# Kernel optimization log

Measured on AMD Instinct MI355X. Metric: run time of the kernel, lower is better.

## Reference

```python
import jax, jax.numpy as jnp
import numpy as np

EPS = 1e-6          # module eps for denominator
KERNEL_EPS = 1e-4   # performer softmax_kernel numerical eps


def softmax_kernel(data, projection):
    # data: [n, l, h, e]; projection: [m, e] -> features [n, l, h, m]
    d = data.shape[-1]
    m = projection.shape[0]
    data_normalizer = d ** -0.25
    ratio = m ** -0.5
    data_dash = jnp.einsum('nlhe,me->nlhm', data * data_normalizer, projection)
    diag_data = (0.5 * (data_normalizer ** 2)) * jnp.sum(data * data, axis=-1, keepdims=True)
    # numerically stable exp with per-row max subtraction
    data_dash = ratio * (jnp.exp(data_dash - diag_data - jnp.max(data_dash, axis=-1, keepdims=True)) + KERNEL_EPS)
    return data_dash


def _gaussian_orthogonal_random_matrix(nb_rows, nb_cols, seed=0):
    rng = np.random.default_rng(seed)
    blocks = []
    for _ in range(int(np.ceil(nb_rows / nb_cols))):
        q, _ = np.linalg.qr(rng.standard_normal((nb_cols, nb_cols)))
        blocks.append(q.T)
    proj = np.concatenate(blocks, axis=0)[:nb_rows]
    # scaling=0: chi-distributed row multipliers
    multiplier = np.linalg.norm(rng.standard_normal((nb_rows, nb_cols)), axis=1)
    return (multiplier[:, None] * proj).astype(np.float32)


def setup_inputs() -> dict:
    n, l, h, e = 2, 2048, 8, 64
    nb_features = l  # module: nb_features = l when l >= e
    key = jax.random.key(0)
    kq, kk, kv = jax.random.split(key, 3)
    queries = jax.random.normal(kq, (n, l, h, e), jnp.float32)
    keys = jax.random.normal(kk, (n, l, h, e), jnp.float32)
    values = jax.random.normal(kv, (n, l, h, e), jnp.float32)
    projection = jnp.asarray(_gaussian_orthogonal_random_matrix(nb_features, e))
    return {"queries": queries, "keys": keys, "values": values, "projection": projection}


def reference(queries, keys, values, projection):
    # Performer linear attention, batched (bi=None) branch
    q = softmax_kernel(queries, projection)   # [n, l, h, m]
    k = softmax_kernel(keys, projection)      # [n, l, h, m]
    kv = jnp.einsum('nshm,nshe->nhem', k, values)              # [n, h, e, m]
    z = 1.0 / (jnp.einsum('nlhm,nhm->nlh', q, k.sum(axis=1)) + EPS)  # [n, l, h]
    v = jnp.einsum('nlhm,nhem,nlh->nlhe', q, kv, z)             # [n, l, h, e]
    return v
```

## Files before the change

kernel.cpp:

```cpp
#include <hip/hip_runtime.h>


#define LL 2048
#define HH 8
#define MM 2048
#define ROWSTR 512

#define NORMC 0.35355339059327373f
#define RATIO 0.022097086912079608f
#define KEPS 1e-4f
#define REPS (RATIO * KEPS)
#define EPSD 1e-6f

#define KVSPLIT 2097152
#define RSPLIT 32768

typedef __attribute__((ext_vector_type(8))) short short8;
typedef __attribute__((ext_vector_type(4))) float f32x4;

#define MFMA(a, b, c) __builtin_amdgcn_mfma_f32_16x16x32_bf16((a), (b), (c), 0, 0, 0)

__device__ __forceinline__ unsigned short f2bf(float f) {
    union { float f; unsigned int u; } v; v.f = f;
    unsigned int r = v.u + 0x7fffu + ((v.u >> 16) & 1u);
    return (unsigned short)(r >> 16);
}
__device__ __forceinline__ float bf2f(unsigned short u) {
    union { unsigned int ui; float f; } v; v.ui = ((unsigned int)u) << 16; return v.f;
}
__device__ __forceinline__ unsigned int pk2(float lo, float hi) {
    return __builtin_amdgcn_perm(__float_as_uint(hi), __float_as_uint(lo), 0x07060302u);
}

template <bool BF16>
__device__ __forceinline__ void tile_load(const void* src, size_t base, size_t rstride,
                                          int t, uint4& A, uint4& B) {
    const int row = t >> 2, c16 = (t & 3) * 16;
    if (BF16) {
        const unsigned short* p = (const unsigned short*)src + base + (size_t)row * rstride + c16;
        A = *(const uint4*)p;
        B = *(const uint4*)(p + 8);
    } else {
        const float* p = (const float*)src + base + (size_t)row * rstride + c16;
        float4 f0 = ((const float4*)p)[0], f1 = ((const float4*)p)[1];
        float4 f2 = ((const float4*)p)[2], f3 = ((const float4*)p)[3];
        A.x = pk2(f0.x, f0.y); A.y = pk2(f0.z, f0.w);
        A.z = pk2(f1.x, f1.y); A.w = pk2(f1.z, f1.w);
        B.x = pk2(f2.x, f2.y); B.y = pk2(f2.z, f2.w);
        B.z = pk2(f3.x, f3.y); B.w = pk2(f3.z, f3.w);
    }
}
__device__ __forceinline__ void tile_store(unsigned short D[64][72], int t, uint4 A, uint4 B) {
    const int row = t >> 2, c16 = (t & 3) * 16;
    *(uint4*)&D[row][c16] = A;
    *(uint4*)&D[row][c16 + 8] = B;
}

template <bool BF16>
__device__ __forceinline__ void vt_load(const void* V, size_t base, int t, uint4& A, uint4& B) {
    const int s0 = (t & 31) * 2, e0 = (t >> 5) * 8;
    if (BF16) {
        const unsigned short* p = (const unsigned short*)V + base + (size_t)s0 * ROWSTR + e0;
        A = *(const uint4*)p;
        B = *(const uint4*)(p + ROWSTR);
    } else {
        const float* p = (const float*)V + base + (size_t)s0 * ROWSTR + e0;
        float4 f0 = ((const float4*)p)[0], f1 = ((const float4*)p)[1];
        const float* q = p + ROWSTR;
        float4 g0 = ((const float4*)q)[0], g1 = ((const float4*)q)[1];
        A.x = pk2(f0.x, f0.y); A.y = pk2(f0.z, f0.w);
        A.z = pk2(f1.x, f1.y); A.w = pk2(f1.z, f1.w);
        B.x = pk2(g0.x, g0.y); B.y = pk2(g0.z, g0.w);
        B.z = pk2(g1.x, g1.y); B.w = pk2(g1.z, g1.w);
    }
}
__device__ __forceinline__ void vt_store(unsigned short VT[64][72], int t, uint4 A, uint4 B) {
    const int s0 = (t & 31) * 2, e0 = (t >> 5) * 8;
    const unsigned ua[4] = {A.x, A.y, A.z, A.w}, ub[4] = {B.x, B.y, B.z, B.w};
    #pragma unroll
    for (int i = 0; i < 4; ++i) {
        *(unsigned*)&VT[e0 + 2 * i][s0] = (ua[i] & 0xFFFFu) | (ub[i] << 16);
        *(unsigned*)&VT[e0 + 2 * i + 1][s0] = (ua[i] >> 16) | (ub[i] & 0xFFFF0000u);
    }
}

__device__ __forceinline__ void kv2_load(const float* kvf01, size_t base, int t, float4 R[8]) {
    const int m0 = (t & 31) * 2, e0 = (t >> 5) * 8;
    const float* p = kvf01 + base + (size_t)m0 * 64 + e0;
    R[0] = ((const float4*)p)[0];        R[1] = ((const float4*)p)[1];
    R[2] = ((const float4*)(p + 64))[0]; R[3] = ((const float4*)(p + 64))[1];
    const float* q = p + KVSPLIT;
    R[4] = ((const float4*)q)[0];        R[5] = ((const float4*)q)[1];
    R[6] = ((const float4*)(q + 64))[0]; R[7] = ((const float4*)(q + 64))[1];
}
__device__ __forceinline__ void kv2_store(unsigned short D[64][72], int t, const float4 R[8]) {
    const int m0 = (t & 31) * 2, e0 = (t >> 5) * 8;
    const float r0[8] = {R[0].x + R[4].x, R[0].y + R[4].y, R[0].z + R[4].z, R[0].w + R[4].w,
                         R[1].x + R[5].x, R[1].y + R[5].y, R[1].z + R[5].z, R[1].w + R[5].w};
    const float r1[8] = {R[2].x + R[6].x, R[2].y + R[6].y, R[2].z + R[6].z, R[2].w + R[6].w,
                         R[3].x + R[7].x, R[3].y + R[7].y, R[3].z + R[7].z, R[3].w + R[7].w};
    #pragma unroll
    for (int i = 0; i < 8; ++i)
        *(unsigned*)&D[e0 + i][m0] = (unsigned)f2bf(r0[i]) | ((unsigned)f2bf(r1[i]) << 16);
}

__global__ void LinearAttention_15985868276494_detect(const unsigned short* __restrict__ P,
                                                      float* __restrict__ flag) {
    if (threadIdx.x == 0) {
        int sane = 1;
        #pragma unroll
        for (int i = 0; i < 16; ++i) {
            const unsigned e = (P[2 * i] >> 7) & 0xFF;
            if (e < 101 || e > 141) sane = 0;
        }
        *flag = sane ? 1.0f : 0.0f;
    }
}

template <bool BF16>
__device__ void stats_impl(const void* X, const void* P, float* cws,
                           unsigned short Xs[64][72], unsigned short Ps[2][64][72],
                           float* diag_s) {
    const int t = threadIdx.x;
    const int w = t >> 6, ln = t & 15, quad = (t >> 4) & 3;
    const int row_base = blockIdx.x * 64;

    {
        uint4 xa, xb;
        tile_load<BF16>(X, (size_t)row_base * 64, 64, t, xa, xb);
        tile_store(Xs, t, xa, xb);
        uint4 pa, pb;
        tile_load<BF16>(P, 0, 64, t, pa, pb);
        tile_store(Ps[0], t, pa, pb);
    }
    __syncthreads();
    if (t < 64) {
        float s2 = 0.f;
        #pragma unroll
        for (int c = 0; c < 64; c += 8) {
            uint4 u = *(const uint4*)&Xs[t][c];
            const unsigned int ua[4] = {u.x, u.y, u.z, u.w};
            #pragma unroll
            for (int i = 0; i < 4; ++i) {
                float lo = bf2f((unsigned short)(ua[i] & 0xFFFF));
                float hi = bf2f((unsigned short)(ua[i] >> 16));
                s2 = fmaf(lo, lo, s2); s2 = fmaf(hi, hi, s2);
            }
        }
        diag_s[t] = s2;
    }
    const short8 xb0 = *(const short8*)&Xs[16 * w + ln][quad * 8];
    const short8 xb1 = *(const short8*)&Xs[16 * w + ln][32 + quad * 8];

    uint4 pfa, pfb;
    tile_load<BF16>(P, (size_t)64 * 64, 64, t, pfa, pfb);

    float rmax = -3.0e38f;
    for (int mt = 0; mt < 32; ++mt) {
        const int cur = mt & 1;
        __syncthreads();
        if (mt + 1 < 32) {
            tile_store(Ps[cur ^ 1], t, pfa, pfb);
            if (mt + 2 < 32)
                tile_load<BF16>(P, (size_t)((mt + 2) * 64) * 64, 64, t, pfa, pfb);
        }
        #pragma unroll
        for (int ms = 0; ms < 4; ++ms) {
            f32x4 acc = {0.f, 0.f, 0.f, 0.f};
            acc = MFMA(*(const short8*)&Ps[cur][16 * ms + ln][quad * 8], xb0, acc);
            acc = MFMA(*(const short8*)&Ps[cur][16 * ms + ln][32 + quad * 8], xb1, acc);
            rmax = fmaxf(rmax, fmaxf(fmaxf(acc[0], acc[1]), fmaxf(acc[2], acc[3])));
        }
    }
    rmax = fmaxf(rmax, __shfl_xor(rmax, 16));
    rmax = fmaxf(rmax, __shfl_xor(rmax, 32));
    __syncthreads();
    if ((t & 63) < 16) {
        const int row = 16 * w + ln;
        const int rg = row_base + row;
        const int n = rg >> 14, l = (rg >> 3) & 2047, h = rg & 7;
        cws[(size_t)((n << 3) | h) * LL + l] =
            NORMC * rmax + (0.5f * NORMC * NORMC) * diag_s[row];
    }
}

__global__ __launch_bounds__(256) void LinearAttention_15985868276494_stats(
        const void* K, const void* Q, const void* P, const float* flag,
        float* c_k, float* c_q) {
    __shared__ unsigned short Xs[64][72];
    __shared__ unsigned short Ps[2][64][72];
    __shared__ float diag_s[64];
    const void* X = (blockIdx.y == 0) ? K : Q;
    float* cws = (blockIdx.y == 0) ? c_k : c_q;
    if (*flag != 0.f) stats_impl<true>(X, P, cws, Xs, Ps, diag_s);
    else stats_impl<false>(X, P, cws, Xs, Ps, diag_s);
}

template <bool BF16>
__device__ void kv_impl(const void* K, const void* V, const void* P, const float* cws,
                        float* kvf01, float* ksum01,
                        unsigned short Ks[2][64][72], unsigned short VT[2][64][72],
                        unsigned short Ps[64][72], unsigned short FT[64][72],
                        float cks[2][64]) {
    const int t = threadIdx.x;
    const int w = t >> 6, ln = t & 15, quad = (t >> 4) & 3;
    const int mt = blockIdx.x, nh = blockIdx.y, sp = blockIdx.z;
    const int n = nh >> 3, h = nh & 7;
    const size_t xbase = (size_t)n * (LL * ROWSTR) + (size_t)h * 64;
    const int st0 = sp * 16;

    {
        uint4 pa, pb;
        tile_load<BF16>(P, (size_t)(mt * 64) * 64, 64, t, pa, pb);
        tile_store(Ps, t, pa, pb);
    }
    uint4 kA, kB, vA, vB;
    float ckr = 0.f;
    tile_load<BF16>(K, xbase + (size_t)(st0 * 64) * ROWSTR, ROWSTR, t, kA, kB);
    vt_load<BF16>(V, xbase + (size_t)(st0 * 64) * ROWSTR, t, vA, vB);
    if (t < 64) ckr = cws[(size_t)nh * LL + st0 * 64 + t];
    tile_store(Ks[0], t, kA, kB);
    vt_store(VT[0], t, vA, vB);
    if (t < 64) cks[0][t] = ckr;
    tile_load<BF16>(K, xbase + (size_t)((st0 + 1) * 64) * ROWSTR, ROWSTR, t, kA, kB);
    vt_load<BF16>(V, xbase + (size_t)((st0 + 1) * 64) * ROWSTR, t, vA, vB);
    if (t < 64) ckr = cws[(size_t)nh * LL + (st0 + 1) * 64 + t];
    __syncthreads();

    const short8 pb0 = *(const short8*)&Ps[16 * w + ln][quad * 8];
    const short8 pb1 = *(const short8*)&Ps[16 * w + ln][32 + quad * 8];
    f32x4 akv[4] = {{0.f, 0.f, 0.f, 0.f}, {0.f, 0.f, 0.f, 0.f},
                    {0.f, 0.f, 0.f, 0.f}, {0.f, 0.f, 0.f, 0.f}};
    f32x4 aks = {0.f, 0.f, 0.f, 0.f};
    const short8 ones = {0x3F80, 0x3F80, 0x3F80, 0x3F80, 0x3F80, 0x3F80, 0x3F80, 0x3F80};

    for (int i = 0; i < 16; ++i) {
        const int cur = i & 1;
        if (i + 1 < 16) {
            tile_store(Ks[cur ^ 1], t, kA, kB);
            vt_store(VT[cur ^ 1], t, vA, vB);
            if (t < 64) cks[cur ^ 1][t] = ckr;
            if (i + 2 < 16) {
                const int st = st0 + i + 2;
                tile_load<BF16>(K, xbase + (size_t)(st * 64) * ROWSTR, ROWSTR, t, kA, kB);
                vt_load<BF16>(V, xbase + (size_t)(st * 64) * ROWSTR, t, vA, vB);
                if (t < 64) ckr = cws[(size_t)nh * LL + st * 64 + t];
            }
        }
        #pragma unroll
        for (int ss = 0; ss < 4; ++ss) {
            f32x4 acc = {0.f, 0.f, 0.f, 0.f};
            acc = MFMA(*(const short8*)&Ks[cur][16 * ss + ln][quad * 8], pb0, acc);
            acc = MFMA(*(const short8*)&Ks[cur][16 * ss + ln][32 + quad * 8], pb1, acc);
            const float4 c4 = *(const float4*)&cks[cur][16 * ss + 4 * quad];
            const float ca[4] = {c4.x, c4.y, c4.z, c4.w};
            float f[4];
            #pragma unroll
            for (int j = 0; j < 4; ++j) {
                const float arg = fminf(fmaf(acc[j], NORMC, -ca[j]), 0.f);
                f[j] = fmaf(__expf(arg), RATIO, REPS);
            }
            uint2 o; o.x = pk2(f[0], f[1]); o.y = pk2(f[2], f[3]);
            *(uint2*)&FT[16 * w + ln][16 * ss + 4 * quad] = o;
        }
        #pragma unroll
        for (int k = 0; k < 2; ++k) {
            const short8 af = *(const short8*)&FT[16 * w + ln][32 * k + quad * 8];
            aks = MFMA(af, ones, aks);
            #pragma unroll
            for (int es = 0; es < 4; ++es)
                akv[es] = MFMA(af, *(const short8*)&VT[cur][16 * es + ln][32 * k + quad * 8],
                               akv[es]);
        }
        __syncthreads();
    }
    float* kvfp = kvf01 + (size_t)sp * KVSPLIT + (size_t)nh * (MM * 64);
    #pragma unroll
    for (int r = 0; r < 4; ++r) {
        const int m = mt * 64 + 16 * w + 4 * quad + r;
        #pragma unroll
        for (int es = 0; es < 4; ++es)
            kvfp[(size_t)m * 64 + 16 * es + ln] = akv[es][r];
        if (ln == 0)
            ksum01[(size_t)sp * RSPLIT + (size_t)nh * MM + m] = aks[r];
    }
}

__global__ __launch_bounds__(256) void LinearAttention_15985868276494_kv(
        const void* K, const void* V, const void* P, const float* flag,
        const float* cws, float* kvf01, float* ksum01) {
    __shared__ unsigned short Ks[2][64][72];
    __shared__ unsigned short VT[2][64][72];
    __shared__ unsigned short Ps[64][72];
    __shared__ unsigned short FT[64][72];
    __shared__ float cks[2][64];
    if (*flag != 0.f) kv_impl<true>(K, V, P, cws, kvf01, ksum01, Ks, VT, Ps, FT, cks);
    else kv_impl<false>(K, V, P, cws, kvf01, ksum01, Ks, VT, Ps, FT, cks);
}

__global__ __launch_bounds__(256) void LinearAttention_15985868276494_reduce(
        const float* __restrict__ kvf01, const float* __restrict__ ksum01,
        unsigned short* __restrict__ kvT, float* __restrict__ ksum) {
    __shared__ unsigned short T[64][72];
    const int t = threadIdx.x;
    const int mt = blockIdx.x, nh = blockIdx.y;
    float4 R[8];
    kv2_load(kvf01, (size_t)nh * (MM * 64) + (size_t)(mt * 64) * 64, t, R);
    kv2_store(T, t, R);
    if (t < 64)
        ksum[(size_t)nh * MM + mt * 64 + t] =
            ksum01[(size_t)nh * MM + mt * 64 + t] +
            ksum01[RSPLIT + (size_t)nh * MM + mt * 64 + t];
    __syncthreads();
    const int e = t >> 2, c = (t & 3) * 16;
    uint4 a = *(const uint4*)&T[e][c];
    uint4 b = *(const uint4*)&T[e][c + 8];
    unsigned short* dst = kvT + ((size_t)nh * 64 + e) * MM + mt * 64 + c;
    *(uint4*)dst = a;
    *(uint4*)(dst + 8) = b;
}

template <bool BF16>
__device__ void out_impl(const void* Q, const void* P, const float* cqw,
                         const unsigned short* kvT, const float* ksum, void* out,
                         unsigned short Qs[64][72], unsigned short Ps[2][64][72],
                         unsigned short KVs[2][64][72], unsigned short Fs[64][72],
                         unsigned short kss[2][72]) {
    const int t = threadIdx.x;
    const int w = t >> 6, ln = t & 15, quad = (t >> 4) & 3;
    const int lb = blockIdx.x, nh = blockIdx.y;
    const int n = nh >> 3, h = nh & 7;
    const size_t qbase = (size_t)n * (LL * ROWSTR) + (size_t)h * 64 + (size_t)(lb * 64) * ROWSTR;
    const size_t kvbase = (size_t)nh * (size_t)(64 * MM);

    {
        uint4 qa, qb;
        tile_load<BF16>(Q, qbase, ROWSTR, t, qa, qb);
        tile_store(Qs, t, qa, qb);
    }
    uint4 pA, pB, kA, kB;
    float ksr = 0.f;
    tile_load<BF16>(P, 0, 64, t, pA, pB);
    tile_load<true>(kvT, kvbase, MM, t, kA, kB);
    if (t < 64) ksr = ksum[(size_t)nh * MM + t];
    tile_store(Ps[0], t, pA, pB);
    tile_store(KVs[0], t, kA, kB);
    if (t < 64) kss[0][t] = f2bf(ksr);
    tile_load<BF16>(P, (size_t)64 * 64, 64, t, pA, pB);
    tile_load<true>(kvT, kvbase + 64, MM, t, kA, kB);
    if (t < 64) ksr = ksum[(size_t)nh * MM + 64 + t];
    __syncthreads();

    const short8 qb0 = *(const short8*)&Qs[16 * w + ln][quad * 8];
    const short8 qb1 = *(const short8*)&Qs[16 * w + ln][32 + quad * 8];
    const float cq = cqw[(size_t)nh * LL + lb * 64 + 16 * w + ln];

    f32x4 ao[4] = {{0.f, 0.f, 0.f, 0.f}, {0.f, 0.f, 0.f, 0.f},
                   {0.f, 0.f, 0.f, 0.f}, {0.f, 0.f, 0.f, 0.f}};
    f32x4 ad = {0.f, 0.f, 0.f, 0.f};

    for (int mt = 0; mt < 32; ++mt) {
        const int cur = mt & 1;
        if (mt + 1 < 32) {
            tile_store(Ps[cur ^ 1], t, pA, pB);
            tile_store(KVs[cur ^ 1], t, kA, kB);
            if (t < 64) kss[cur ^ 1][t] = f2bf(ksr);
            if (mt + 2 < 32) {
                tile_load<BF16>(P, (size_t)((mt + 2) * 64) * 64, 64, t, pA, pB);
                tile_load<true>(kvT, kvbase + (mt + 2) * 64, MM, t, kA, kB);
                if (t < 64) ksr = ksum[(size_t)nh * MM + (mt + 2) * 64 + t];
            }
        }
        #pragma unroll
        for (int ms = 0; ms < 4; ++ms) {
            f32x4 acc = {0.f, 0.f, 0.f, 0.f};
            acc = MFMA(*(const short8*)&Ps[cur][16 * ms + ln][quad * 8], qb0, acc);
            acc = MFMA(*(const short8*)&Ps[cur][16 * ms + ln][32 + quad * 8], qb1, acc);
            float f[4];
            #pragma unroll
            for (int j = 0; j < 4; ++j) {
                const float arg = fminf(fmaf(acc[j], NORMC, -cq), 0.f);
                f[j] = fmaf(__expf(arg), RATIO, REPS);
            }
            uint2 o; o.x = pk2(f[0], f[1]); o.y = pk2(f[2], f[3]);
            *(uint2*)&Fs[16 * w + ln][16 * ms + 4 * quad] = o;
        }
        #pragma unroll
        for (int k = 0; k < 2; ++k) {
            const short8 af = *(const short8*)&Fs[16 * w + ln][32 * k + quad * 8];
            const short8 bs = *(const short8*)&kss[cur][32 * k + quad * 8];
            ad = MFMA(af, bs, ad);
            #pragma unroll
            for (int es = 0; es < 4; ++es)
                ao[es] = MFMA(af, *(const short8*)&KVs[cur][16 * es + ln][32 * k + quad * 8],
                              ao[es]);
        }
        __syncthreads();
    }
    float z[4];
    #pragma unroll
    for (int r = 0; r < 4; ++r) z[r] = 1.0f / (ad[r] + EPSD);
    #pragma unroll
    for (int r = 0; r < 4; ++r) {
        const int l = lb * 64 + 16 * w + 4 * quad + r;
        const size_t rowoff = ((size_t)(n * LL + l) * HH + h) * 64;
        #pragma unroll
        for (int es = 0; es < 4; ++es) {
            const float val = ao[es][r] * z[r];
            if (BF16) ((unsigned short*)out)[rowoff + 16 * es + ln] = f2bf(val);
            else ((float*)out)[rowoff + 16 * es + ln] = val;
        }
    }
}

__global__ __launch_bounds__(256) void LinearAttention_15985868276494_out(
        const void* Q, const void* P, const float* flag, const float* cqw,
        const unsigned short* kvT, const float* ksum, void* out) {
    __shared__ unsigned short Qs[64][72];
    __shared__ unsigned short Ps[2][64][72];
    __shared__ unsigned short KVs[2][64][72];
    __shared__ unsigned short Fs[64][72];
    __shared__ unsigned short kss[2][72];
    if (*flag != 0.f) out_impl<true>(Q, P, cqw, kvT, ksum, out, Qs, Ps, KVs, Fs, kss);
    else out_impl<false>(Q, P, cqw, kvT, ksum, out, Qs, Ps, KVs, Fs, kss);
}

extern "C" void kernel_launch(void* const* d_in, const int* in_sizes, int n_in,
                              void* d_out, int out_size, void* d_ws, size_t ws_size,
                              hipStream_t stream) {
    const void* Q = d_in[0];
    const void* K = d_in[1];
    const void* V = d_in[2];
    const void* P = d_in[3];

    float* W = (float*)d_ws;
    float* flag = W;
    float* c_k = W + 16;
    float* c_q = c_k + 32768;
    float* ksum01 = c_q + 32768;
    float* kvf01 = ksum01 + 2 * RSPLIT;
    float* ksumW = kvf01 + 2 * KVSPLIT;
    unsigned short* kvTW = (unsigned short*)(ksumW + RSPLIT);

    LinearAttention_15985868276494_detect<<<1, 64, 0, stream>>>(
        (const unsigned short*)P, flag);
    LinearAttention_15985868276494_stats<<<dim3(512, 2), 256, 0, stream>>>(
        K, Q, P, flag, c_k, c_q);
    LinearAttention_15985868276494_kv<<<dim3(32, 16, 2), 256, 0, stream>>>(
        K, V, P, flag, c_k, kvf01, ksum01);
    LinearAttention_15985868276494_reduce<<<dim3(32, 16), 256, 0, stream>>>(
        kvf01, ksum01, kvTW, ksumW);
    LinearAttention_15985868276494_out<<<dim3(32, 16), 256, 0, stream>>>(
        Q, P, flag, c_q, kvTW, ksumW, d_out);
}
```

Measured before the change: 214.6 us.

## Switch all GEMM stages to 32x32x16 MFMA with register-shuffled feature fragments

Replaces the 16x16x32 bf16 MFMA tiling with 32x32x16 MFMA across the stats, kv and output kernels. The exp feature tile now stays in registers and is passed to the next MFMA through lane-xor shuffles instead of a shared-memory round trip. The stats kernel processes 128 rows per block, and the output kernel splits work across waves, reducing partial results through shared memory in an epilogue that writes vectorized stores. Launch bounds, dynamic shared memory sizes and the reduce grid change to match. The aim is fewer MFMA issues, fewer LDS accesses and fewer barriers, in exchange for more register pressure and a more complex cross-wave reduction.

```diff
diff --git a/kernel.cpp b/kernel.cpp
--- a/kernel.cpp
+++ b/kernel.cpp
@@ -16,20 +16,26 @@
 #define RSPLIT 32768
 
 typedef __attribute__((ext_vector_type(8))) short short8;
-typedef __attribute__((ext_vector_type(4))) float f32x4;
-
-#define MFMA(a, b, c) __builtin_amdgcn_mfma_f32_16x16x32_bf16((a), (b), (c), 0, 0, 0)
-
+typedef __attribute__((ext_vector_type(16))) float f32x16;
+
+#define MFMA32(a, b, c) __builtin_amdgcn_mfma_f32_32x32x16_bf16((a), (b), (c), 0, 0, 0)
+
+__device__ __forceinline__ f32x16 zero16() {
+    f32x16 v;
+    #pragma unroll
+    for (int i = 0; i < 16; ++i) v[i] = 0.f;
+    return v;
+}
 __device__ __forceinline__ unsigned short f2bf(float f) {
     union { float f; unsigned int u; } v; v.f = f;
     unsigned int r = v.u + 0x7fffu + ((v.u >> 16) & 1u);
     return (unsigned short)(r >> 16);
 }
+__device__ __forceinline__ unsigned int pk2(float lo, float hi) {
+    return __builtin_amdgcn_perm(__float_as_uint(hi), __float_as_uint(lo), 0x07060302u);
+}
 __device__ __forceinline__ float bf2f(unsigned short u) {
     union { unsigned int ui; float f; } v; v.ui = ((unsigned int)u) << 16; return v.f;
-}
-__device__ __forceinline__ unsigned int pk2(float lo, float hi) {
-    return __builtin_amdgcn_perm(__float_as_uint(hi), __float_as_uint(lo), 0x07060302u);
 }
 
 template <bool BF16>
@@ -50,10 +56,10 @@
         B.z = pk2(f3.x, f3.y); B.w = pk2(f3.z, f3.w);
     }
 }
-__device__ __forceinline__ void tile_store(unsigned short D[64][72], int t, uint4 A, uint4 B) {
+__device__ __forceinline__ void tile_store72(unsigned short* D, int t, uint4 A, uint4 B) {
     const int row = t >> 2, c16 = (t & 3) * 16;
-    *(uint4*)&D[row][c16] = A;
-    *(uint4*)&D[row][c16 + 8] = B;
+    *(uint4*)&D[row * 72 + c16] = A;
+    *(uint4*)&D[row * 72 + c16 + 8] = B;
 }
 
 template <bool BF16>
@@ -74,34 +80,27 @@
         B.z = pk2(g1.x, g1.y); B.w = pk2(g1.z, g1.w);
     }
 }
-__device__ __forceinline__ void vt_store(unsigned short VT[64][72], int t, uint4 A, uint4 B) {
+__device__ __forceinline__ void vt_store72(unsigned short* VT, int t, uint4 A, uint4 B) {
     const int s0 = (t & 31) * 2, e0 = (t >> 5) * 8;
     const unsigned ua[4] = {A.x, A.y, A.z, A.w}, ub[4] = {B.x, B.y, B.z, B.w};
     #pragma unroll
     for (int i = 0; i < 4; ++i) {
-        *(unsigned*)&VT[e0 + 2 * i][s0] = (ua[i] & 0xFFFFu) | (ub[i] << 16);
-        *(unsigned*)&VT[e0 + 2 * i + 1][s0] = (ua[i] >> 16) | (ub[i] & 0xFFFF0000u);
-    }
-}
-
-__device__ __forceinline__ void kv2_load(const float* kvf01, size_t base, int t, float4 R[8]) {
-    const int m0 = (t & 31) * 2, e0 = (t >> 5) * 8;
-    const float* p = kvf01 + base + (size_t)m0 * 64 + e0;
-    R[0] = ((const float4*)p)[0];        R[1] = ((const float4*)p)[1];
-    R[2] = ((const float4*)(p + 64))[0]; R[3] = ((const float4*)(p + 64))[1];
-    const float* q = p + KVSPLIT;
-    R[4] = ((const float4*)q)[0];        R[5] = ((const float4*)q)[1];
-    R[6] = ((const float4*)(q + 64))[0]; R[7] = ((const float4*)(q + 64))[1];
-}
-__device__ __forceinline__ void kv2_store(unsigned short D[64][72], int t, const float4 R[8]) {
-    const int m0 = (t & 31) * 2, e0 = (t >> 5) * 8;
-    const float r0[8] = {R[0].x + R[4].x, R[0].y + R[4].y, R[0].z + R[4].z, R[0].w + R[4].w,
-                         R[1].x + R[5].x, R[1].y + R[5].y, R[1].z + R[5].z, R[1].w + R[5].w};
-    const float r1[8] = {R[2].x + R[6].x, R[2].y + R[6].y, R[2].z + R[6].z, R[2].w + R[6].w,
-                         R[3].x + R[7].x, R[3].y + R[7].y, R[3].z + R[7].z, R[3].w + R[7].w};
-    #pragma unroll
-    for (int i = 0; i < 8; ++i)
-        *(unsigned*)&D[e0 + i][m0] = (unsigned)f2bf(r0[i]) | ((unsigned)f2bf(r1[i]) << 16);
+        *(unsigned*)&VT[(e0 + 2 * i) * 72 + s0] = (ua[i] & 0xFFFFu) | (ub[i] << 16);
+        *(unsigned*)&VT[(e0 + 2 * i + 1) * 72 + s0] = (ua[i] >> 16) | (ub[i] & 0xFFFF0000u);
+    }
+}
+
+__device__ __forceinline__ short8 xfrag(const unsigned int pd[8], int cp, int hi) {
+    const unsigned int s0 = hi ? pd[4 * cp + 0] : pd[4 * cp + 2];
+    const unsigned int s1 = hi ? pd[4 * cp + 1] : pd[4 * cp + 3];
+    const unsigned int r0 = (unsigned int)__shfl_xor((int)s0, 32);
+    const unsigned int r1 = (unsigned int)__shfl_xor((int)s1, 32);
+    union { unsigned int u[4]; short8 s; } v;
+    v.u[0] = hi ? r0 : pd[4 * cp + 0];
+    v.u[1] = hi ? r1 : pd[4 * cp + 1];
+    v.u[2] = hi ? pd[4 * cp + 2] : r0;
+    v.u[3] = hi ? pd[4 * cp + 3] : r1;
+    return v.s;
 }
 
 __global__ void LinearAttention_15985868276494_detect(const unsigned short* __restrict__ P,
@@ -119,127 +118,149 @@
 
 template <bool BF16>
 __device__ void stats_impl(const void* X, const void* P, float* cws,
-                           unsigned short Xs[64][72], unsigned short Ps[2][64][72],
-                           float* diag_s) {
+                           unsigned short* Xs, unsigned short* Ps, float* red) {
     const int t = threadIdx.x;
-    const int w = t >> 6, ln = t & 15, quad = (t >> 4) & 3;
-    const int row_base = blockIdx.x * 64;
-
-    {
-        uint4 xa, xb;
-        tile_load<BF16>(X, (size_t)row_base * 64, 64, t, xa, xb);
-        tile_store(Xs, t, xa, xb);
-        uint4 pa, pb;
-        tile_load<BF16>(P, 0, 64, t, pa, pb);
-        tile_store(Ps[0], t, pa, pb);
-    }
+    const int w = t >> 6, ln = t & 31, hi = (t >> 5) & 1;
+    const int row_base = blockIdx.x * 128;
+
+    uint4 a0, b0, a1, b1;
+    tile_load<BF16>(X, (size_t)row_base * 64, 64, t, a0, b0);
+    tile_store72(Xs, t, a0, b0);
+    tile_load<BF16>(X, (size_t)(row_base + 64) * 64, 64, t, a1, b1);
+    tile_store72(Xs + 64 * 72, t, a1, b1);
+    tile_load<BF16>(P, 0, 64, t, a0, b0);
+    tile_store72(Ps, t, a0, b0);
+    tile_load<BF16>(P, (size_t)64 * 64, 64, t, a1, b1);
+    tile_store72(Ps + 64 * 72, t, a1, b1);
+    uint4 pA0, pB0, pA1, pB1;
+    tile_load<BF16>(P, (size_t)128 * 64, 64, t, pA0, pB0);
+    tile_load<BF16>(P, (size_t)192 * 64, 64, t, pA1, pB1);
     __syncthreads();
-    if (t < 64) {
+
+    short8 xb[4][4];
+    #pragma unroll
+    for (int xs = 0; xs < 4; ++xs)
+        #pragma unroll
+        for (int c = 0; c < 4; ++c)
+            xb[xs][c] = *(const short8*)&Xs[(32 * xs + ln) * 72 + 16 * c + 8 * hi];
+
+    float rmax4[4] = {-3e38f, -3e38f, -3e38f, -3e38f};
+    for (int mt = 0; mt < 16; ++mt) {
+        const int cur = mt & 1;
+        unsigned short* Pc = Ps + cur * (128 * 72);
+        if (mt + 1 < 16) {
+            unsigned short* Pn = Ps + (cur ^ 1) * (128 * 72);
+            tile_store72(Pn, t, pA0, pB0);
+            tile_store72(Pn + 64 * 72, t, pA1, pB1);
+            if (mt + 2 < 16) {
+                tile_load<BF16>(P, (size_t)((mt + 2) * 128) * 64, 64, t, pA0, pB0);
+                tile_load<BF16>(P, (size_t)((mt + 2) * 128 + 64) * 64, 64, t, pA1, pB1);
+            }
+        }
+        #pragma unroll
+        for (int xs = 0; xs < 4; ++xs) {
+            f32x16 acc = zero16();
+            #pragma unroll
+            for (int c = 0; c < 4; ++c) {
+                const short8 af = *(const short8*)&Pc[(32 * w + ln) * 72 + 16 * c + 8 * hi];
+                acc = MFMA32(af, xb[xs][c], acc);
+            }
+            float m = acc[0];
+            #pragma unroll
+            for (int r = 1; r < 16; ++r) m = fmaxf(m, acc[r]);
+            rmax4[xs] = fmaxf(rmax4[xs], m);
+        }
+        __syncthreads();
+    }
+    #pragma unroll
+    for (int xs = 0; xs < 4; ++xs) {
+        const float m = fmaxf(rmax4[xs], __shfl_xor(rmax4[xs], 32));
+        if (hi == 0) red[w * 128 + xs * 32 + ln] = m;
+    }
+    __syncthreads();
+    if (t < 128) {
+        const float rm = fmaxf(fmaxf(red[t], red[128 + t]), fmaxf(red[256 + t], red[384 + t]));
         float s2 = 0.f;
         #pragma unroll
         for (int c = 0; c < 64; c += 8) {
-            uint4 u = *(const uint4*)&Xs[t][c];
+            uint4 u = *(const uint4*)&Xs[t * 72 + c];
             const unsigned int ua[4] = {u.x, u.y, u.z, u.w};
             #pragma unroll
             for (int i = 0; i < 4; ++i) {
-                float lo = bf2f((unsigned short)(ua[i] & 0xFFFF));
-                float hi = bf2f((unsigned short)(ua[i] >> 16));
-                s2 = fmaf(lo, lo, s2); s2 = fmaf(hi, hi, s2);
-            }
-        }
-        diag_s[t] = s2;
-    }
-    const short8 xb0 = *(const short8*)&Xs[16 * w + ln][quad * 8];
-    const short8 xb1 = *(const short8*)&Xs[16 * w + ln][32 + quad * 8];
-
-    uint4 pfa, pfb;
-    tile_load<BF16>(P, (size_t)64 * 64, 64, t, pfa, pfb);
-
-    float rmax = -3.0e38f;
-    for (int mt = 0; mt < 32; ++mt) {
-        const int cur = mt & 1;
-        __syncthreads();
-        if (mt + 1 < 32) {
-            tile_store(Ps[cur ^ 1], t, pfa, pfb);
-            if (mt + 2 < 32)
-                tile_load<BF16>(P, (size_t)((mt + 2) * 64) * 64, 64, t, pfa, pfb);
-        }
-        #pragma unroll
-        for (int ms = 0; ms < 4; ++ms) {
-            f32x4 acc = {0.f, 0.f, 0.f, 0.f};
-            acc = MFMA(*(const short8*)&Ps[cur][16 * ms + ln][quad * 8], xb0, acc);
-            acc = MFMA(*(const short8*)&Ps[cur][16 * ms + ln][32 + quad * 8], xb1, acc);
-            rmax = fmaxf(rmax, fmaxf(fmaxf(acc[0], acc[1]), fmaxf(acc[2], acc[3])));
-        }
-    }
-    rmax = fmaxf(rmax, __shfl_xor(rmax, 16));
-    rmax = fmaxf(rmax, __shfl_xor(rmax, 32));
-    __syncthreads();
-    if ((t & 63) < 16) {
-        const int row = 16 * w + ln;
-        const int rg = row_base + row;
+                const float lo = bf2f((unsigned short)(ua[i] & 0xFFFF));
+                const float hv = bf2f((unsigned short)(ua[i] >> 16));
+                s2 = fmaf(lo, lo, s2); s2 = fmaf(hv, hv, s2);
+            }
+        }
+        const int rg = row_base + t;
         const int n = rg >> 14, l = (rg >> 3) & 2047, h = rg & 7;
-        cws[(size_t)((n << 3) | h) * LL + l] =
-            NORMC * rmax + (0.5f * NORMC * NORMC) * diag_s[row];
-    }
-}
-
-__global__ __launch_bounds__(256) void LinearAttention_15985868276494_stats(
+        cws[(size_t)((n << 3) | h) * LL + l] = NORMC * rm + (0.5f * NORMC * NORMC) * s2;
+    }
+}
+
+__global__ __launch_bounds__(256, 2) void LinearAttention_15985868276494_stats(
         const void* K, const void* Q, const void* P, const float* flag,
         float* c_k, float* c_q) {
-    __shared__ unsigned short Xs[64][72];
-    __shared__ unsigned short Ps[2][64][72];
-    __shared__ float diag_s[64];
+    __shared__ unsigned short Xs[128 * 72];
+    __shared__ unsigned short Ps[2 * 128 * 72];
+    __shared__ float red[512];
     const void* X = (blockIdx.y == 0) ? K : Q;
     float* cws = (blockIdx.y == 0) ? c_k : c_q;
-    if (*flag != 0.f) stats_impl<true>(X, P, cws, Xs, Ps, diag_s);
-    else stats_impl<false>(X, P, cws, Xs, Ps, diag_s);
+    if (*flag != 0.f) stats_impl<true>(X, P, cws, Xs, Ps, red);
+    else stats_impl<false>(X, P, cws, Xs, Ps, red);
 }
 
 template <bool BF16>
 __device__ void kv_impl(const void* K, const void* V, const void* P, const float* cws,
-                        float* kvf01, float* ksum01,
-                        unsigned short Ks[2][64][72], unsigned short VT[2][64][72],
-                        unsigned short Ps[64][72], unsigned short FT[64][72],
-                        float cks[2][64]) {
+                        float* kvf01, float* ksum01, char* smem) {
+    unsigned short* Ks = (unsigned short*)smem;
+    unsigned short* VT = (unsigned short*)(smem + 18432);
+    unsigned short* Ps = (unsigned short*)(smem + 36864);
+    float* cks = (float*)(smem + 46080);
+    float* fin = (float*)smem;
+
     const int t = threadIdx.x;
-    const int w = t >> 6, ln = t & 15, quad = (t >> 4) & 3;
+    const int w = t >> 6, ln = t & 31, hi = (t >> 5) & 1;
+    const int sstrip = w & 1, mstrip = w >> 1;
     const int mt = blockIdx.x, nh = blockIdx.y, sp = blockIdx.z;
     const int n = nh >> 3, h = nh & 7;
     const size_t xbase = (size_t)n * (LL * ROWSTR) + (size_t)h * 64;
     const int st0 = sp * 16;
 
     {
-        uint4 pa, pb;
-        tile_load<BF16>(P, (size_t)(mt * 64) * 64, 64, t, pa, pb);
-        tile_store(Ps, t, pa, pb);
-    }
-    uint4 kA, kB, vA, vB;
-    float ckr = 0.f;
+        uint4 pa, pbv;
+        tile_load<BF16>(P, (size_t)(mt * 64) * 64, 64, t, pa, pbv);
+        tile_store72(Ps, t, pa, pbv);
+    }
+    uint4 kA, kB, vA, vB; float ckr = 0.f;
     tile_load<BF16>(K, xbase + (size_t)(st0 * 64) * ROWSTR, ROWSTR, t, kA, kB);
     vt_load<BF16>(V, xbase + (size_t)(st0 * 64) * ROWSTR, t, vA, vB);
     if (t < 64) ckr = cws[(size_t)nh * LL + st0 * 64 + t];
-    tile_store(Ks[0], t, kA, kB);
-    vt_store(VT[0], t, vA, vB);
-    if (t < 64) cks[0][t] = ckr;
+    tile_store72(Ks, t, kA, kB);
+    vt_store72(VT, t, vA, vB);
+    if (t < 64) cks[t] = ckr;
     tile_load<BF16>(K, xbase + (size_t)((st0 + 1) * 64) * ROWSTR, ROWSTR, t, kA, kB);
     vt_load<BF16>(V, xbase + (size_t)((st0 + 1) * 64) * ROWSTR, t, vA, vB);
     if (t < 64) ckr = cws[(size_t)nh * LL + (st0 + 1) * 64 + t];
     __syncthreads();
 
-    const short8 pb0 = *(const short8*)&Ps[16 * w + ln][quad * 8];
-    const short8 pb1 = *(const short8*)&Ps[16 * w + ln][32 + quad * 8];
-    f32x4 akv[4] = {{0.f, 0.f, 0.f, 0.f}, {0.f, 0.f, 0.f, 0.f},
-                    {0.f, 0.f, 0.f, 0.f}, {0.f, 0.f, 0.f, 0.f}};
-    f32x4 aks = {0.f, 0.f, 0.f, 0.f};
+    short8 pb[4];
+    #pragma unroll
+    for (int c = 0; c < 4; ++c)
+        pb[c] = *(const short8*)&Ps[(32 * mstrip + ln) * 72 + 16 * c + 8 * hi];
     const short8 ones = {0x3F80, 0x3F80, 0x3F80, 0x3F80, 0x3F80, 0x3F80, 0x3F80, 0x3F80};
+
+    f32x16 akv0 = zero16(), akv1 = zero16(), aks = zero16();
 
     for (int i = 0; i < 16; ++i) {
         const int cur = i & 1;
+        unsigned short* Kc = Ks + cur * 4608;
+        unsigned short* Vc = VT + cur * 4608;
+        const float* cc = cks + cur * 64;
         if (i + 1 < 16) {
-            tile_store(Ks[cur ^ 1], t, kA, kB);
-            vt_store(VT[cur ^ 1], t, vA, vB);
-            if (t < 64) cks[cur ^ 1][t] = ckr;
+            tile_store72(Ks + (cur ^ 1) * 4608, t, kA, kB);
+            vt_store72(VT + (cur ^ 1) * 4608, t, vA, vB);
+            if (t < 64) cks[(cur ^ 1) * 64 + t] = ckr;
             if (i + 2 < 16) {
                 const int st = st0 + i + 2;
                 tile_load<BF16>(K, xbase + (size_t)(st * 64) * ROWSTR, ROWSTR, t, kA, kB);
@@ -247,182 +268,248 @@
                 if (t < 64) ckr = cws[(size_t)nh * LL + st * 64 + t];
             }
         }
-        #pragma unroll
-        for (int ss = 0; ss < 4; ++ss) {
-            f32x4 acc = {0.f, 0.f, 0.f, 0.f};
-            acc = MFMA(*(const short8*)&Ks[cur][16 * ss + ln][quad * 8], pb0, acc);
-            acc = MFMA(*(const short8*)&Ks[cur][16 * ss + ln][32 + quad * 8], pb1, acc);
-            const float4 c4 = *(const float4*)&cks[cur][16 * ss + 4 * quad];
+        f32x16 D = zero16();
+        #pragma unroll
+        for (int c = 0; c < 4; ++c) {
+            const short8 af = *(const short8*)&Kc[(32 * sstrip + ln) * 72 + 16 * c + 8 * hi];
+            D = MFMA32(af, pb[c], D);
+        }
+        unsigned int pd[8];
+        #pragma unroll
+        for (int g = 0; g < 4; ++g) {
+            const float4 c4 = *(const float4*)&cc[32 * sstrip + 8 * g + 4 * hi];
             const float ca[4] = {c4.x, c4.y, c4.z, c4.w};
             float f[4];
             #pragma unroll
-            for (int j = 0; j < 4; ++j) {
-                const float arg = fminf(fmaf(acc[j], NORMC, -ca[j]), 0.f);
-                f[j] = fmaf(__expf(arg), RATIO, REPS);
-            }
-            uint2 o; o.x = pk2(f[0], f[1]); o.y = pk2(f[2], f[3]);
-            *(uint2*)&FT[16 * w + ln][16 * ss + 4 * quad] = o;
-        }
-        #pragma unroll
-        for (int k = 0; k < 2; ++k) {
-            const short8 af = *(const short8*)&FT[16 * w + ln][32 * k + quad * 8];
-            aks = MFMA(af, ones, aks);
-            #pragma unroll
-            for (int es = 0; es < 4; ++es)
-                akv[es] = MFMA(af, *(const short8*)&VT[cur][16 * es + ln][32 * k + quad * 8],
-                               akv[es]);
+            for (int b = 0; b < 4; ++b) {
+                const float arg = fminf(fmaf(D[4 * g + b], NORMC, -ca[b]), 0.f);
+                f[b] = fmaf(__expf(arg), RATIO, REPS);
+            }
+            pd[2 * g] = pk2(f[0], f[1]);
+            pd[2 * g + 1] = pk2(f[2], f[3]);
+        }
+        #pragma unroll
+        for (int cp = 0; cp < 2; ++cp) {
+            const short8 bf = xfrag(pd, cp, hi);
+            const int scol = 32 * sstrip + 16 * cp + 8 * hi;
+            const short8 v0 = *(const short8*)&Vc[ln * 72 + scol];
+            const short8 v1 = *(const short8*)&Vc[(32 + ln) * 72 + scol];
+            akv0 = MFMA32(v0, bf, akv0);
+            akv1 = MFMA32(v1, bf, akv1);
+            aks = MFMA32(ones, bf, aks);
         }
         __syncthreads();
     }
-    float* kvfp = kvf01 + (size_t)sp * KVSPLIT + (size_t)nh * (MM * 64);
-    #pragma unroll
-    for (int r = 0; r < 4; ++r) {
-        const int m = mt * 64 + 16 * w + 4 * quad + r;
-        #pragma unroll
-        for (int es = 0; es < 4; ++es)
-            kvfp[(size_t)m * 64 + 16 * es + ln] = akv[es][r];
-        if (ln == 0)
-            ksum01[(size_t)sp * RSPLIT + (size_t)nh * MM + m] = aks[r];
-    }
-}
-
-__global__ __launch_bounds__(256) void LinearAttention_15985868276494_kv(
+    {
+        const int slot = (w * 64 + (t & 63)) * 36;
+        #pragma unroll
+        for (int r = 0; r < 16; ++r) fin[slot + r] = akv0[r];
+        #pragma unroll
+        for (int r = 0; r < 16; ++r) fin[slot + 16 + r] = akv1[r];
+        fin[slot + 32] = aks[0];
+    }
+    __syncthreads();
+    {
+        const int e = t >> 2;
+        const int t16 = e >> 5, e5 = e & 31;
+        const int hi_s = (e5 >> 2) & 1;
+        const int reg = 16 * t16 + (e5 & 3) + 4 * (e5 >> 3);
+        float* dst = kvf01 + (size_t)sp * KVSPLIT + (size_t)nh * (64 * MM)
+                   + (size_t)e * MM + mt * 64 + (t & 3) * 16;
+        #pragma unroll
+        for (int jq = 0; jq < 4; ++jq) {
+            float o[4];
+            #pragma unroll
+            for (int b = 0; b < 4; ++b) {
+                const int m_local = (t & 3) * 16 + 4 * jq + b;
+                const int ms = m_local >> 5;
+                const int lane_s = hi_s * 32 + (m_local & 31);
+                o[b] = fin[((2 * ms) * 64 + lane_s) * 36 + reg]
+                     + fin[((2 * ms + 1) * 64 + lane_s) * 36 + reg];
+            }
+            *(float4*)&dst[4 * jq] = make_float4(o[0], o[1], o[2], o[3]);
+        }
+        if (t < 64) {
+            const int ms = t >> 5;
+            const float val = fin[((2 * ms) * 64 + (t & 31)) * 36 + 32]
+                            + fin[((2 * ms + 1) * 64 + (t & 31)) * 36 + 32];
+            ksum01[(size_t)sp * RSPLIT + (size_t)nh * MM + mt * 64 + t] = val;
+        }
+    }
+}
+
+__global__ __launch_bounds__(256, 3) void LinearAttention_15985868276494_kv(
         const void* K, const void* V, const void* P, const float* flag,
         const float* cws, float* kvf01, float* ksum01) {
-    __shared__ unsigned short Ks[2][64][72];
-    __shared__ unsigned short VT[2][64][72];
-    __shared__ unsigned short Ps[64][72];
-    __shared__ unsigned short FT[64][72];
-    __shared__ float cks[2][64];
-    if (*flag != 0.f) kv_impl<true>(K, V, P, cws, kvf01, ksum01, Ks, VT, Ps, FT, cks);
-    else kv_impl<false>(K, V, P, cws, kvf01, ksum01, Ks, VT, Ps, FT, cks);
+    extern __shared__ char smem_kv[];
+    if (*flag != 0.f) kv_impl<true>(K, V, P, cws, kvf01, ksum01, smem_kv);
+    else kv_impl<false>(K, V, P, cws, kvf01, ksum01, smem_kv);
 }
 
 __global__ __launch_bounds__(256) void LinearAttention_15985868276494_reduce(
         const float* __restrict__ kvf01, const float* __restrict__ ksum01,
-        unsigned short* __restrict__ kvT, float* __restrict__ ksum) {
-    __shared__ unsigned short T[64][72];
-    const int t = threadIdx.x;
-    const int mt = blockIdx.x, nh = blockIdx.y;
-    float4 R[8];
-    kv2_load(kvf01, (size_t)nh * (MM * 64) + (size_t)(mt * 64) * 64, t, R);
-    kv2_store(T, t, R);
-    if (t < 64)
-        ksum[(size_t)nh * MM + mt * 64 + t] =
-            ksum01[(size_t)nh * MM + mt * 64 + t] +
-            ksum01[RSPLIT + (size_t)nh * MM + mt * 64 + t];
-    __syncthreads();
-    const int e = t >> 2, c = (t & 3) * 16;
-    uint4 a = *(const uint4*)&T[e][c];
-    uint4 b = *(const uint4*)&T[e][c + 8];
-    unsigned short* dst = kvT + ((size_t)nh * 64 + e) * MM + mt * 64 + c;
-    *(uint4*)dst = a;
-    *(uint4*)(dst + 8) = b;
+        unsigned short* __restrict__ kvT, float* __restrict__ ksumW) {
+    const int gid = blockIdx.x * 256 + threadIdx.x;
+    const size_t i4 = (size_t)gid * 4;
+    const float4 a = *(const float4*)&kvf01[i4];
+    const float4 b = *(const float4*)&kvf01[KVSPLIT + i4];
+    uint2 o;
+    o.x = (unsigned)f2bf(a.x + b.x) | ((unsigned)f2bf(a.y + b.y) << 16);
+    o.y = (unsigned)f2bf(a.z + b.z) | ((unsigned)f2bf(a.w + b.w) << 16);
+    *(uint2*)&kvT[i4] = o;
+    if (blockIdx.x < 32) {
+        const float4 c = *(const float4*)&ksum01[i4];
+        const float4 d = *(const float4*)&ksum01[RSPLIT + i4];
+        *(float4*)&ksumW[i4] = make_float4(c.x + d.x, c.y + d.y, c.z + d.z, c.w + d.w);
+    }
 }
 
 template <bool BF16>
 __device__ void out_impl(const void* Q, const void* P, const float* cqw,
-                         const unsigned short* kvT, const float* ksum, void* out,
-                         unsigned short Qs[64][72], unsigned short Ps[2][64][72],
-                         unsigned short KVs[2][64][72], unsigned short Fs[64][72],
-                         unsigned short kss[2][72]) {
+                         const unsigned short* kvT, const float* ksum, void* outp,
+                         char* smem) {
+    unsigned short* Qs = (unsigned short*)smem;
+    unsigned short* Ps = (unsigned short*)(smem + 9216);
+    unsigned short* KVs = (unsigned short*)(smem + 27648);
+    unsigned short* kss = (unsigned short*)(smem + 46080);
+    float* fin = (float*)(smem + 9216);
+
     const int t = threadIdx.x;
-    const int w = t >> 6, ln = t & 15, quad = (t >> 4) & 3;
+    const int w = t >> 6, ln = t & 31, hi = (t >> 5) & 1;
+    const int mstrip = w & 1, lstrip = w >> 1;
     const int lb = blockIdx.x, nh = blockIdx.y;
     const int n = nh >> 3, h = nh & 7;
     const size_t qbase = (size_t)n * (LL * ROWSTR) + (size_t)h * 64 + (size_t)(lb * 64) * ROWSTR;
     const size_t kvbase = (size_t)nh * (size_t)(64 * MM);
 
     {
-        uint4 qa, qb;
-        tile_load<BF16>(Q, qbase, ROWSTR, t, qa, qb);
-        tile_store(Qs, t, qa, qb);
-    }
-    uint4 pA, pB, kA, kB;
-    float ksr = 0.f;
+        uint4 qa, qbv;
+        tile_load<BF16>(Q, qbase, ROWSTR, t, qa, qbv);
+        tile_store72(Qs, t, qa, qbv);
+    }
+    uint4 pA, pB, kA, kB; float ksr = 0.f;
     tile_load<BF16>(P, 0, 64, t, pA, pB);
     tile_load<true>(kvT, kvbase, MM, t, kA, kB);
     if (t < 64) ksr = ksum[(size_t)nh * MM + t];
-    tile_store(Ps[0], t, pA, pB);
-    tile_store(KVs[0], t, kA, kB);
-    if (t < 64) kss[0][t] = f2bf(ksr);
+    tile_store72(Ps, t, pA, pB);
+    tile_store72(KVs, t, kA, kB);
+    if (t < 64) kss[t] = f2bf(ksr);
     tile_load<BF16>(P, (size_t)64 * 64, 64, t, pA, pB);
     tile_load<true>(kvT, kvbase + 64, MM, t, kA, kB);
     if (t < 64) ksr = ksum[(size_t)nh * MM + 64 + t];
     __syncthreads();
 
-    const short8 qb0 = *(const short8*)&Qs[16 * w + ln][quad * 8];
-    const short8 qb1 = *(const short8*)&Qs[16 * w + ln][32 + quad * 8];
-    const float cq = cqw[(size_t)nh * LL + lb * 64 + 16 * w + ln];
-
-    f32x4 ao[4] = {{0.f, 0.f, 0.f, 0.f}, {0.f, 0.f, 0.f, 0.f},
-                   {0.f, 0.f, 0.f, 0.f}, {0.f, 0.f, 0.f, 0.f}};
-    f32x4 ad = {0.f, 0.f, 0.f, 0.f};
+    short8 qb[4];
+    #pragma unroll
+    for (int c = 0; c < 4; ++c)
+        qb[c] = *(const short8*)&Qs[(32 * lstrip + ln) * 72 + 16 * c + 8 * hi];
+    const float cq = cqw[(size_t)nh * LL + lb * 64 + lstrip * 32 + ln];
+
+    f32x16 ao0 = zero16(), ao1 = zero16(), ad = zero16();
 
     for (int mt = 0; mt < 32; ++mt) {
         const int cur = mt & 1;
+        unsigned short* Pc = Ps + cur * 4608;
+        unsigned short* Kc = KVs + cur * 4608;
+        const unsigned short* ksc = kss + cur * 64;
         if (mt + 1 < 32) {
-            tile_store(Ps[cur ^ 1], t, pA, pB);
-            tile_store(KVs[cur ^ 1], t, kA, kB);
-            if (t < 64) kss[cur ^ 1][t] = f2bf(ksr);
+            tile_store72(Ps + (cur ^ 1) * 4608, t, pA, pB);
+            tile_store72(KVs + (cur ^ 1) * 4608, t, kA, kB);
+            if (t < 64) kss[(cur ^ 1) * 64 + t] = f2bf(ksr);
             if (mt + 2 < 32) {
                 tile_load<BF16>(P, (size_t)((mt + 2) * 64) * 64, 64, t, pA, pB);
                 tile_load<true>(kvT, kvbase + (mt + 2) * 64, MM, t, kA, kB);
                 if (t < 64) ksr = ksum[(size_t)nh * MM + (mt + 2) * 64 + t];
             }
         }
-        #pragma unroll
-        for (int ms = 0; ms < 4; ++ms) {
-            f32x4 acc = {0.f, 0.f, 0.f, 0.f};
-            acc = MFMA(*(const short8*)&Ps[cur][16 * ms + ln][quad * 8], qb0, acc);
-            acc = MFMA(*(const short8*)&Ps[cur][16 * ms + ln][32 + quad * 8], qb1, acc);
+        f32x16 D = zero16();
+        #pragma unroll
+        for (int c = 0; c < 4; ++c) {
+            const short8 af = *(const short8*)&Pc[(32 * mstrip + ln) * 72 + 16 * c + 8 * hi];
+            D = MFMA32(af, qb[c], D);
+        }
+        unsigned int pd[8];
+        #pragma unroll
+        for (int g = 0; g < 4; ++g) {
             float f[4];
             #pragma unroll
-            for (int j = 0; j < 4; ++j) {
-                const float arg = fminf(fmaf(acc[j], NORMC, -cq), 0.f);
-                f[j] = fmaf(__expf(arg), RATIO, REPS);
-            }
-            uint2 o; o.x = pk2(f[0], f[1]); o.y = pk2(f[2], f[3]);
-            *(uint2*)&Fs[16 * w + ln][16 * ms + 4 * quad] = o;
-        }
-        #pragma unroll
-        for (int k = 0; k < 2; ++k) {
-            const short8 af = *(const short8*)&Fs[16 * w + ln][32 * k + quad * 8];
-            const short8 bs = *(const short8*)&kss[cur][32 * k + quad * 8];
-            ad = MFMA(af, bs, ad);
-            #pragma unroll
-            for (int es = 0; es < 4; ++es)
-                ao[es] = MFMA(af, *(const short8*)&KVs[cur][16 * es + ln][32 * k + quad * 8],
-                              ao[es]);
+            for (int b = 0; b < 4; ++b) {
+                const float arg = fminf(fmaf(D[4 * g + b], NORMC, -cq), 0.f);
+                f[b] = fmaf(__expf(arg), RATIO, REPS);
+            }
+            pd[2 * g] = pk2(f[0], f[1]);
+            pd[2 * g + 1] = pk2(f[2], f[3]);
+        }
+        #pragma unroll
+        for (int cp = 0; cp < 2; ++cp) {
+            const short8 bf = xfrag(pd, cp, hi);
+            const int mcol = 32 * mstrip + 16 * cp + 8 * hi;
+            const short8 a0 = *(const short8*)&Kc[ln * 72 + mcol];
+            const short8 a1 = *(const short8*)&Kc[(32 + ln) * 72 + mcol];
+            const short8 k8 = *(const short8*)&ksc[mcol];
+            ao0 = MFMA32(a0, bf, ao0);
+            ao1 = MFMA32(a1, bf, ao1);
+            ad = MFMA32(k8, bf, ad);
         }
         __syncthreads();
     }
-    float z[4];
-    #pragma unroll
-    for (int r = 0; r < 4; ++r) z[r] = 1.0f / (ad[r] + EPSD);
-    #pragma unroll
-    for (int r = 0; r < 4; ++r) {
-        const int l = lb * 64 + 16 * w + 4 * quad + r;
-        const size_t rowoff = ((size_t)(n * LL + l) * HH + h) * 64;
-        #pragma unroll
-        for (int es = 0; es < 4; ++es) {
-            const float val = ao[es][r] * z[r];
-            if (BF16) ((unsigned short*)out)[rowoff + 16 * es + ln] = f2bf(val);
-            else ((float*)out)[rowoff + 16 * es + ln] = val;
-        }
-    }
-}
-
-__global__ __launch_bounds__(256) void LinearAttention_15985868276494_out(
+    {
+        const int slot = (w * 64 + (t & 63)) * 36;
+        #pragma unroll
+        for (int r = 0; r < 16; ++r) fin[slot + r] = ao0[r];
+        #pragma unroll
+        for (int r = 0; r < 16; ++r) fin[slot + 16 + r] = ao1[r];
+        fin[slot + 32] = ad[0];
+    }
+    __syncthreads();
+    {
+        const int l_local = t >> 2, eg = t & 3;
+        const int ls = l_local >> 5, lane_l = l_local & 31;
+        const float adt = fin[((2 * ls) * 64 + lane_l) * 36 + 32]
+                        + fin[((2 * ls + 1) * 64 + lane_l) * 36 + 32];
+        const float z = 1.0f / (adt + EPSD);
+        const int l = lb * 64 + l_local;
+        const size_t rowoff = ((size_t)(n * LL + l) * HH + h) * 64 + eg * 16;
+        float vals[16];
+        #pragma unroll
+        for (int j = 0; j < 16; ++j) {
+            const int e = eg * 16 + j;
+            const int t16 = e >> 5, e5 = e & 31;
+            const int hi_s = (e5 >> 2) & 1;
+            const int reg = 16 * t16 + (e5 & 3) + 4 * (e5 >> 3);
+            const int lane_s = hi_s * 32 + lane_l;
+            vals[j] = (fin[((2 * ls) * 64 + lane_s) * 36 + reg]
+                     + fin[((2 * ls + 1) * 64 + lane_s) * 36 + reg]) * z;
+        }
+        if (BF16) {
+            uint4 o0, o1;
+            o0.x = (unsigned)f2bf(vals[0]) | ((unsigned)f2bf(vals[1]) << 16);
+            o0.y = (unsigned)f2bf(vals[2]) | ((unsigned)f2bf(vals[3]) << 16);
+            o0.z = (unsigned)f2bf(vals[4]) | ((unsigned)f2bf(vals[5]) << 16);
+            o0.w = (unsigned)f2bf(vals[6]) | ((unsigned)f2bf(vals[7]) << 16);
+            o1.x = (unsigned)f2bf(vals[8]) | ((unsigned)f2bf(vals[9]) << 16);
+            o1.y = (unsigned)f2bf(vals[10]) | ((unsigned)f2bf(vals[11]) << 16);
+            o1.z = (unsigned)f2bf(vals[12]) | ((unsigned)f2bf(vals[13]) << 16);
+            o1.w = (unsigned)f2bf(vals[14]) | ((unsigned)f2bf(vals[15]) << 16);
+            unsigned short* op = (unsigned short*)outp + rowoff;
+            *(uint4*)op = o0;
+            *(uint4*)(op + 8) = o1;
+        } else {
+            float* op = (float*)outp + rowoff;
+            #pragma unroll
+            for (int q4 = 0; q4 < 4; ++q4)
+                *(float4*)&op[4 * q4] = make_float4(vals[4 * q4], vals[4 * q4 + 1],
+                                                    vals[4 * q4 + 2], vals[4 * q4 + 3]);
+        }
+    }
+}
+
+__global__ __launch_bounds__(256, 3) void LinearAttention_15985868276494_out(
         const void* Q, const void* P, const float* flag, const float* cqw,
-        const unsigned short* kvT, const float* ksum, void* out) {
-    __shared__ unsigned short Qs[64][72];
-    __shared__ unsigned short Ps[2][64][72];
-    __shared__ unsigned short KVs[2][64][72];
-    __shared__ unsigned short Fs[64][72];
-    __shared__ unsigned short kss[2][72];
-    if (*flag != 0.f) out_impl<true>(Q, P, cqw, kvT, ksum, out, Qs, Ps, KVs, Fs, kss);
-    else out_impl<false>(Q, P, cqw, kvT, ksum, out, Qs, Ps, KVs, Fs, kss);
+        const unsigned short* kvT, const float* ksum, void* outp) {
+    extern __shared__ char smem_out[];
+    if (*flag != 0.f) out_impl<true>(Q, P, cqw, kvT, ksum, outp, smem_out);
+    else out_impl<false>(Q, P, cqw, kvT, ksum, outp, smem_out);
 }
 
 extern "C" void kernel_launch(void* const* d_in, const int* in_sizes, int n_in,
@@ -444,12 +531,12 @@
 
     LinearAttention_15985868276494_detect<<<1, 64, 0, stream>>>(
         (const unsigned short*)P, flag);
-    LinearAttention_15985868276494_stats<<<dim3(512, 2), 256, 0, stream>>>(
+    LinearAttention_15985868276494_stats<<<dim3(256, 2), 256, 0, stream>>>(
         K, Q, P, flag, c_k, c_q);
-    LinearAttention_15985868276494_kv<<<dim3(32, 16, 2), 256, 0, stream>>>(
+    LinearAttention_15985868276494_kv<<<dim3(32, 16, 2), 256, 46592, stream>>>(
         K, V, P, flag, c_k, kvf01, ksum01);
-    LinearAttention_15985868276494_reduce<<<dim3(32, 16), 256, 0, stream>>>(
+    LinearAttention_15985868276494_reduce<<<2048, 256, 0, stream>>>(
         kvf01, ksum01, kvTW, ksumW);
-    LinearAttention_15985868276494_out<<<dim3(32, 16), 256, 0, stream>>>(
+    LinearAttention_15985868276494_out<<<dim3(32, 16), 256, 46592, stream>>>(
         Q, P, flag, c_q, kvTW, ksumW, d_out);
 }
```

New measurement: 191.5 us. -10.8%, faster.
